# Performance work log

Measured on AMD Instinct MI355X. Metric: run time of the kernel, lower is better.

## Reference

```python
import jax, jax.numpy as jnp
import numpy as np

B, R, C = 256, 1024, 1024
N_IDX = 64


def setup_inputs() -> dict:
    key = jax.random.key(0)
    kx, = jax.random.split(key, 1)
    x = jax.random.normal(kx, (B, R, C), dtype=jnp.float32)
    rows = jnp.arange(N_IDX, dtype=jnp.int32)
    cols = jnp.arange(N_IDX, dtype=jnp.int32)
    return {"x": x, "rows": rows, "cols": cols}


def _mute_msb(x):
    # frexp: x = m * 2**e with m in [0.5, 1). Muting the MSB of the exponent
    # (per the original: e = 0 if e > 0 else e) multiplies x by 2**(min(e,0)-e),
    # i.e. scales by 2**(-e) when e > 0, identity otherwise.
    e = jnp.frexp(x)[1]                                   # int exponent
    e = jax.lax.stop_gradient(e)
    scale = jnp.where(e > 0, jnp.exp2(-e.astype(x.dtype)), jnp.ones_like(x))
    return x * scale


def reference(x, rows, cols):
    # Boolean mask over the [R, C] plane selecting the (rows x cols) grid.
    mask = jnp.zeros((x.shape[1], x.shape[2]), dtype=bool)
    mask = mask.at[rows[:, None], cols[None, :]].set(True)
    y = _mute_msb(x)
    # Apply only on the selected grid, broadcast over batch.
    return jnp.where(mask[None, :, :], y, x)
```

## Files before the change

kernel.cpp:

```cpp
#include <hip/hip_runtime.h>
#include <hip/hip_bf16.h>


#define RR 1024
#define CC 1024

typedef float f4 __attribute__((ext_vector_type(4)));

__global__ void build_masks_kernel(const int* __restrict__ rows,
                                   const int* __restrict__ cols,
                                   unsigned* __restrict__ masks,
                                   int nr, int nc) {
    int t = threadIdx.x;
    if (t < 64) masks[t] = 0u;
    __syncthreads();
    if (t < nr) {
        int r = rows[t];
        atomicOr(&masks[r >> 5], 1u << (r & 31));
    }
    if (t < nc) {
        int c = cols[t];
        atomicOr(&masks[32 + (c >> 5)], 1u << (c & 31));
    }
}

__device__ __forceinline__ void mute4(f4& v, unsigned m) {
#pragma unroll
    for (int k = 0; k < 4; ++k) {
        if ((m >> k) & 1u) {
            unsigned u = __float_as_uint(v[k]);
            unsigned E = (u >> 23) & 0xffu;
            if (E >= 127u && E < 255u)
                v[k] = __uint_as_float((u & 0x807fffffu) | (126u << 23));
        }
    }
}

__global__ void copy_mute_kernel(const f4* __restrict__ x,
                                 f4* __restrict__ out,
                                 const unsigned* __restrict__ masks,
                                 int nrows) {
    __shared__ unsigned rowmask[32];
    int tid = threadIdx.x;
    if (tid < 32) rowmask[tid] = masks[tid];
    __syncthreads();

    unsigned colword = masks[32 + (tid >> 3)];
    unsigned colnib = (colword >> ((tid & 7) * 4)) & 0xFu;

    for (int row = blockIdx.x * 2; row < nrows; row += gridDim.x * 2) {
        long long q0 = (long long)row * 256 + tid;
        f4 v0 = __builtin_nontemporal_load(&x[q0]);
        f4 v1 = __builtin_nontemporal_load(&x[q0 + 256]);

        int r0 = row & (RR - 1);
        int r1 = (row + 1) & (RR - 1);
        unsigned m0 = ((rowmask[r0 >> 5] >> (r0 & 31)) & 1u) ? colnib : 0u;
        unsigned m1 = ((rowmask[r1 >> 5] >> (r1 & 31)) & 1u) ? colnib : 0u;

        if (m0) mute4(v0, m0);
        if (m1) mute4(v1, m1);

        __builtin_nontemporal_store(v0, &out[q0]);
        __builtin_nontemporal_store(v1, &out[q0 + 256]);
    }
}

extern "C" void kernel_launch(void* const* d_in, const int* in_sizes, int n_in,
                              void* d_out, int out_size, void* d_ws, size_t ws_size,
                              hipStream_t stream) {
    const float* x  = (const float*)d_in[0];
    const int* rows = (const int*)d_in[1];
    const int* cols = (const int*)d_in[2];
    float* out      = (float*)d_out;
    unsigned* masks = (unsigned*)d_ws;

    const int nr = in_sizes[1];
    const int nc = in_sizes[2];

    build_masks_kernel<<<1, 64, 0, stream>>>(rows, cols, masks, nr, nc);

    int nrows = in_sizes[0] / CC;
    int block = 256;
    int grid = 4096;
    copy_mute_kernel<<<grid, block, 0, stream>>>(
        (const f4*)x, (f4*)out, masks, nrows);
}
```

Baseline: 399.6 us.

## Double-buffer loads with four-row unroll and hoist per-thread row masks

The copy kernel now processes four rows per iteration and alternates two register buffers, so the next iteration's loads are issued before the current rows are muted and stored. Row-mask bits are computed once per thread, relying on the grid stride being a multiple of the row count per plane. This aims to keep more memory requests in flight in a bandwidth-bound copy, at the cost of higher register use. It also depends on the stride aligning with the 1024-row plane.

Result: faster. 374.3 us (-6.3%).

```diff
diff --git a/kernel.cpp b/kernel.cpp
--- a/kernel.cpp
+++ b/kernel.cpp
@@ -4,6 +4,7 @@
 
 #define RR 1024
 #define CC 1024
+#define UNROLL 4
 
 typedef float f4 __attribute__((ext_vector_type(4)));
 
@@ -36,10 +37,22 @@
     }
 }
 
-__global__ void copy_mute_kernel(const f4* __restrict__ x,
-                                 f4* __restrict__ out,
-                                 const unsigned* __restrict__ masks,
-                                 int nrows) {
+#define LOADV(V, qq)                                                        \
+    _Pragma("unroll") for (int k = 0; k < UNROLL; ++k)                      \
+        V[k] = __builtin_nontemporal_load(&x[(qq) + k * 256]);
+
+#define PSTOREV(V, qq)                                                      \
+    _Pragma("unroll") for (int k = 0; k < UNROLL; ++k) {                    \
+        f4 t = V[k];                                                        \
+        if (rb[k]) mute4(t, mnib[k]);                                       \
+        __builtin_nontemporal_store(t, &out[(qq) + k * 256]);               \
+    }
+
+__global__ void __launch_bounds__(256)
+copy_mute_kernel(const f4* __restrict__ x,
+                 f4* __restrict__ out,
+                 const unsigned* __restrict__ masks,
+                 int nrows) {
     __shared__ unsigned rowmask[32];
     int tid = threadIdx.x;
     if (tid < 32) rowmask[tid] = masks[tid];
@@ -48,22 +61,36 @@
     unsigned colword = masks[32 + (tid >> 3)];
     unsigned colnib = (colword >> ((tid & 7) * 4)) & 0xFu;
 
-    for (int row = blockIdx.x * 2; row < nrows; row += gridDim.x * 2) {
-        long long q0 = (long long)row * 256 + tid;
-        f4 v0 = __builtin_nontemporal_load(&x[q0]);
-        f4 v1 = __builtin_nontemporal_load(&x[q0 + 256]);
+    int row0 = blockIdx.x * UNROLL;
+    if (row0 >= nrows) return;
+    int rowstride = gridDim.x * UNROLL;
+    long long qstride = (long long)rowstride * 256;
 
-        int r0 = row & (RR - 1);
-        int r1 = (row + 1) & (RR - 1);
-        unsigned m0 = ((rowmask[r0 >> 5] >> (r0 & 31)) & 1u) ? colnib : 0u;
-        unsigned m1 = ((rowmask[r1 >> 5] >> (r1 & 31)) & 1u) ? colnib : 0u;
+    bool rb[UNROLL];
+    unsigned mnib[UNROLL];
+#pragma unroll
+    for (int k = 0; k < UNROLL; ++k) {
+        int r = (row0 + k) & (RR - 1);
+        rb[k] = ((rowmask[r >> 5] >> (r & 31)) & 1u) != 0u;
+        mnib[k] = colnib;
+    }
 
-        if (m0) mute4(v0, m0);
-        if (m1) mute4(v1, m1);
+    int iters = (nrows - row0 + rowstride - 1) / rowstride;
+    long long q0 = (long long)row0 * 256 + tid;
 
-        __builtin_nontemporal_store(v0, &out[q0]);
-        __builtin_nontemporal_store(v1, &out[q0 + 256]);
+    f4 A[UNROLL], B[UNROLL];
+    LOADV(A, q0)
+    long long qprev = q0;
+    bool prevA = true;
+    for (int t = 1; t < iters; ++t) {
+        long long qt = qprev + qstride;
+        if (prevA) { LOADV(B, qt) PSTOREV(A, qprev) }
+        else       { LOADV(A, qt) PSTOREV(B, qprev) }
+        prevA = !prevA;
+        qprev = qt;
     }
+    if (prevA) { PSTOREV(A, qprev) }
+    else       { PSTOREV(B, qprev) }
 }
 
 extern "C" void kernel_launch(void* const* d_in, const int* in_sizes, int n_in,
@@ -83,6 +110,7 @@
     int nrows = in_sizes[0] / CC;
     int block = 256;
     int grid = 4096;
+    if (grid * UNROLL > nrows) grid = (nrows + UNROLL - 1) / UNROLL;
     copy_mute_kernel<<<grid, block, 0, stream>>>(
         (const f4*)x, (f4*)out, masks, nrows);
 }
```
